# Optimization experiments

Hardware: AMD Instinct MI355X
Metric: run time of the kernel (lower is better)

## Reference

```python
import jax, jax.numpy as jnp
import numpy as np

N = 100000   # total nodes (users + items)
D = 256      # in_channels == out_channels
E = 1000000  # directed edges
C = 64       # number of clusters


def setup_inputs() -> dict:
    key = jax.random.key(0)
    k1, k2, k3, k4, k5 = jax.random.split(key, 5)
    X = jax.random.normal(k1, (N, D), jnp.float32)
    weight = jax.random.normal(k2, (D, D), jnp.float32) / np.sqrt(D).astype(np.float32)
    bias = jax.random.normal(k3, (D,), jnp.float32) * 0.01
    cluster_assignment = jax.random.randint(k4, (N,), 0, C)
    edge_index = jax.random.randint(k5, (2, E), 0, N)
    return {"X": X, "weight": weight, "bias": bias,
            "cluster_assignment": cluster_assignment, "edge_index": edge_index}


def reference(X, weight, bias, cluster_assignment, edge_index):
    # Per-cluster GCNConv == whole-graph GCNConv restricted to intra-cluster
    # edges (edges crossing clusters are masked out), with self-loops added
    # per node. Clusters with zero intra-cluster edges are skipped and keep
    # the original X (the Python loop `continue`s).
    src, dst = edge_index[0], edge_index[1]
    intra = (cluster_assignment[src] == cluster_assignment[dst]).astype(X.dtype)

    # GCN symmetric normalization with self-loops: deg = A_intra deg + 1
    deg = jax.ops.segment_sum(intra, dst, num_segments=N) + 1.0
    dinv = jax.lax.rsqrt(deg)                      # deg >= 1 always
    norm = dinv[src] * dinv[dst] * intra           # zero on cross-cluster edges

    Xl = X @ weight                                # [N, D] linear transform
    agg = jax.ops.segment_sum(norm[:, None] * Xl[src], dst, num_segments=N)
    agg = agg + (dinv * dinv)[:, None] * Xl        # self-loop contribution
    out = agg + bias

    # Clusters with no internal edges are left untouched by the torch loop.
    edges_per_cluster = jax.ops.segment_sum(intra, cluster_assignment[dst], num_segments=C)
    active = edges_per_cluster[cluster_assignment] > 0  # [N] bool
    return jnp.where(active[:, None], out, X)
```

## Files before the change

### kernel.cpp

```cpp
#include <hip/hip_runtime.h>

#define D 256

typedef float f32x4 __attribute__((ext_vector_type(4)));
typedef _Float16 f16x8 __attribute__((ext_vector_type(8)));

__global__ void k_prepw(const float* __restrict__ W, _Float16* __restrict__ Wp,
                        float* __restrict__ degx, int* __restrict__ activeC,
                        int* __restrict__ bcnt, int N) {
    int idx = blockIdx.x * blockDim.x + threadIdx.x;
    if (idx < N) degx[idx] = 0.0f;
    if (idx < 64) activeC[idx] = 0;
    if (idx < 256 * 32) bcnt[idx] = 0;
    if (idx >= D * D) return;
    int k = idx >> 8, n = idx & 255;
    int ks = k >> 5, kk = k & 31;
    int h = kk >> 3, i = kk & 7;
    int ct = n >> 4, cn = n & 15;
    int lane = h * 16 + cn;
    Wp[(((ks * 16 + ct) * 64 + lane) << 3) + i] = (_Float16)W[idx];
}

__global__ void k_edges(const int* __restrict__ ei, const int* __restrict__ cl,
                        float* __restrict__ degx, int2* __restrict__ elist,
                        int* __restrict__ bcnt, int E) {
    int e = blockIdx.x * blockDim.x + threadIdx.x;
    if (e >= E) return;
    int s = ei[e];
    int d = ei[E + e];
    if (cl[s] == cl[d]) {
        unsafeAtomicAdd(&degx[d], 1.0f);
        int b = blockIdx.x & 255;
        int pos = atomicAdd(&bcnt[b << 5], 1);
        if (pos < 256) elist[(b << 8) + pos] = make_int2(s, d);
    }
}

__global__ void k_init(const float* __restrict__ X, const float* __restrict__ degx,
                       const int* __restrict__ cl, int* __restrict__ activeC,
                       float* __restrict__ out, int N) {
    int i = blockIdx.x * blockDim.x + threadIdx.x;
    int lane = threadIdx.x & 63;
    float dx = 0.0f;
    bool hit = false;
    if (i < N) {
        dx = degx[i];
        hit = dx > 0.0f;
        if (hit) activeC[cl[i]] = 1;
    }
    unsigned long long m = __ballot(hit);
    int base = i - lane;
    while (m) {
        int b = __ffsll((long long)m) - 1;
        m &= m - 1;
        int r = base + b;
        float inv = 1.0f / (__shfl(dx, b) + 1.0f);
        float4 x = *(const float4*)(X + (size_t)r * D + lane * 4);
        x.x *= inv; x.y *= inv; x.z *= inv; x.w *= inv;
        *(float4*)(out + (size_t)r * D + lane * 4) = x;
    }
}

__global__ void k_scatter2(const int2* __restrict__ elist,
                           const int* __restrict__ bcnt,
                           const float* __restrict__ degx,
                           const float* __restrict__ X,
                           float* __restrict__ out) {
    int b = blockIdx.x >> 2;
    int w = ((blockIdx.x & 3) << 2) + (threadIdx.x >> 6);
    int lane = threadIdx.x & 63;
    int cnt = bcnt[b << 5];
    if (cnt > 256) cnt = 256;
    for (int i = w; i < cnt; i += 16) {
        int2 e = elist[(b << 8) + i];
        float norm = rsqrtf((degx[e.x] + 1.0f) * (degx[e.y] + 1.0f));
        float4 xv = *(const float4*)(X + (size_t)e.x * D + lane * 4);
        float* op = out + (size_t)e.y * D + lane * 4;
        unsafeAtomicAdd(op + 0, norm * xv.x);
        unsafeAtomicAdd(op + 1, norm * xv.y);
        unsafeAtomicAdd(op + 2, norm * xv.z);
        unsafeAtomicAdd(op + 3, norm * xv.w);
    }
}

__global__ __launch_bounds__(1024, 4) void k_gemm(
        const _Float16* __restrict__ Wp, const float* __restrict__ bias,
        const float* __restrict__ X, const float* __restrict__ degx,
        const int* __restrict__ cl, const int* __restrict__ activeC,
        float* __restrict__ out, int N) {
    extern __shared__ _Float16 Wl[];
    int tid  = threadIdx.x;
    int lane = tid & 63;
    int wid  = tid >> 6;
    int rA = lane & 15;
    int h  = lane >> 4;
    int cn = lane & 15;

    {
        const char* src = (const char*)Wp + tid * 16;
        #pragma unroll
        for (int it = 0; it < 8; ++it) {
            __builtin_amdgcn_global_load_lds(
                (const __attribute__((address_space(1))) void*)(src + it * 16384),
                (__attribute__((address_space(3))) void*)((char*)Wl + tid * 16 + it * 16384),
                16, 0, 0);
        }
    }
    float bv[16];
    #pragma unroll
    for (int ct = 0; ct < 16; ++ct) bv[ct] = bias[ct * 16 + cn];
    __syncthreads();

    int T = (N + 15) >> 4;
    for (int t = (int)blockIdx.x * 16 + wid; t < T; t += 4096) {
        long r = (long)t * 16 + rA;
        if (r > (long)N - 1) r = (long)N - 1;
        const float* arow = ((degx[r] > 0.0f) ? out : X) + r * D;

        f32x4 acc[16];
        #pragma unroll
        for (int ct = 0; ct < 16; ++ct) acc[ct] = (f32x4){0.f, 0.f, 0.f, 0.f};

        float4 Pa = *(const float4*)(arow + h * 8);
        float4 Pb = *(const float4*)(arow + h * 8 + 4);
        #pragma unroll
        for (int ks = 0; ks < 8; ++ks) {
            float4 a0 = Pa, a1 = Pb;
            if (ks < 7) {
                Pa = *(const float4*)(arow + (ks + 1) * 32 + h * 8);
                Pb = *(const float4*)(arow + (ks + 1) * 32 + h * 8 + 4);
            }
            f16x8 af;
            af[0]=(_Float16)a0.x; af[1]=(_Float16)a0.y; af[2]=(_Float16)a0.z; af[3]=(_Float16)a0.w;
            af[4]=(_Float16)a1.x; af[5]=(_Float16)a1.y; af[6]=(_Float16)a1.z; af[7]=(_Float16)a1.w;
            #pragma unroll
            for (int ct = 0; ct < 16; ++ct) {
                f16x8 wf = *(const f16x8*)&Wl[(((ks * 16 + ct) * 64) + lane) << 3];
                acc[ct] = __builtin_amdgcn_mfma_f32_16x16x32_f16(af, wf, acc[ct], 0, 0, 0);
            }
        }

        #pragma unroll
        for (int j = 0; j < 4; ++j) {
            long rr = (long)t * 16 + h * 4 + j;
            bool ok = rr < (long)N;
            long rc = ok ? rr : (long)N - 1;
            bool act = activeC[cl[rc]] != 0;
            unsigned long long bad = __ballot(!act || !ok);
            float* orow = out + rc * D;
            if (bad == 0ULL) {
                #pragma unroll
                for (int ct = 0; ct < 16; ++ct)
                    orow[ct * 16 + cn] = acc[ct][j] + bv[ct];
            } else if (ok) {
                const float* xrow = X + rc * D;
                #pragma unroll
                for (int ct = 0; ct < 16; ++ct) {
                    float v = acc[ct][j] + bv[ct];
                    if (!act) v = xrow[ct * 16 + cn];
                    orow[ct * 16 + cn] = v;
                }
            }
        }
    }
}

extern "C" void kernel_launch(void* const* d_in, const int* in_sizes, int n_in,
                              void* d_out, int out_size, void* d_ws, size_t ws_size,
                              hipStream_t stream) {
    const float* X    = (const float*)d_in[0];
    const float* W    = (const float*)d_in[1];
    const float* bias = (const float*)d_in[2];
    const int*   cl   = (const int*)d_in[3];
    const int*   ei   = (const int*)d_in[4];
    int N = in_sizes[3];
    int E = in_sizes[4] / 2;
    float* out = (float*)d_out;

    char* ws = (char*)d_ws;
    float* degx = (float*)ws;
    size_t off = ((size_t)N * sizeof(float) + 255) & ~(size_t)255;
    int* activeC = (int*)(ws + off);
    int* bcnt    = (int*)(ws + off + 256);
    int2* elist  = (int2*)(ws + off + 256 + 256 * 32 * sizeof(int));
    size_t off2 = off + 256 + 256 * 32 * sizeof(int) + 256 * 256 * sizeof(int2);
    _Float16* Wp = (_Float16*)(ws + ((off2 + 255) & ~(size_t)255));

    hipFuncSetAttribute((const void*)k_gemm,
                        hipFuncAttributeMaxDynamicSharedMemorySize, 131072);

    int npz = (N > D * D) ? N : D * D;
    k_prepw<<<(npz + 255) / 256, 256, 0, stream>>>(W, Wp, degx, activeC, bcnt, N);
    k_edges<<<(E + 255) / 256, 256, 0, stream>>>(ei, cl, degx, elist, bcnt, E);
    k_init<<<(N + 255) / 256, 256, 0, stream>>>(X, degx, cl, activeC, out, N);
    k_scatter2<<<1024, 256, 0, stream>>>(elist, bcnt, degx, X, out);
    k_gemm<<<256, 1024, 131072, stream>>>(Wp, bias, X, degx, cl, activeC, out, N);
}
```

Measured before the change: 128.9 us.

## Fuse all five stages into one cooperative kernel with grid-wide syncs

Merges the weight prep, edge filtering, init, edge scatter and GEMM stages into a single cooperative kernel launched with 256×1024 threads, separating phases with grid.sync(). Edge processing becomes a grid-stride loop, with the block id serving directly as the elist bucket. This aims to remove the launch overhead and inter-kernel gaps of five separate launches. In exchange, the memory-bound phases run at the lower occupancy that the GEMM's launch bounds and 128KB of LDS allow, and each grid barrier adds synchronisation cost.

```diff
diff --git a/kernel.cpp b/kernel.cpp
--- a/kernel.cpp
+++ b/kernel.cpp
@@ -1,102 +1,97 @@
 #include <hip/hip_runtime.h>
+#include <hip/hip_cooperative_groups.h>
 
 #define D 256
+
+namespace cg = cooperative_groups;
 
 typedef float f32x4 __attribute__((ext_vector_type(4)));
 typedef _Float16 f16x8 __attribute__((ext_vector_type(8)));
 
-__global__ void k_prepw(const float* __restrict__ W, _Float16* __restrict__ Wp,
-                        float* __restrict__ degx, int* __restrict__ activeC,
-                        int* __restrict__ bcnt, int N) {
-    int idx = blockIdx.x * blockDim.x + threadIdx.x;
-    if (idx < N) degx[idx] = 0.0f;
-    if (idx < 64) activeC[idx] = 0;
-    if (idx < 256 * 32) bcnt[idx] = 0;
-    if (idx >= D * D) return;
-    int k = idx >> 8, n = idx & 255;
-    int ks = k >> 5, kk = k & 31;
-    int h = kk >> 3, i = kk & 7;
-    int ct = n >> 4, cn = n & 15;
-    int lane = h * 16 + cn;
-    Wp[(((ks * 16 + ct) * 64 + lane) << 3) + i] = (_Float16)W[idx];
-}
+__global__ __launch_bounds__(1024, 4) void k_fused(
+        const float* __restrict__ W, const float* __restrict__ bias,
+        const float* __restrict__ X, const int* __restrict__ cl,
+        const int* __restrict__ ei, _Float16* __restrict__ Wp,
+        float* __restrict__ degx, int* __restrict__ activeC,
+        int* __restrict__ bcnt, int2* __restrict__ elist,
+        float* __restrict__ out, int E, int N) {
+    extern __shared__ _Float16 Wl[];
+    cg::grid_group grid = cg::this_grid();
+    const int tid  = threadIdx.x;
+    const int bid  = blockIdx.x;
+    const int gtid = bid * 1024 + tid;
+    const int lane = tid & 63;
 
-__global__ void k_edges(const int* __restrict__ ei, const int* __restrict__ cl,
-                        float* __restrict__ degx, int2* __restrict__ elist,
-                        int* __restrict__ bcnt, int E) {
-    int e = blockIdx.x * blockDim.x + threadIdx.x;
-    if (e >= E) return;
-    int s = ei[e];
-    int d = ei[E + e];
-    if (cl[s] == cl[d]) {
-        unsafeAtomicAdd(&degx[d], 1.0f);
-        int b = blockIdx.x & 255;
-        int pos = atomicAdd(&bcnt[b << 5], 1);
-        if (pos < 256) elist[(b << 8) + pos] = make_int2(s, d);
+    if (gtid < N) degx[gtid] = 0.0f;
+    if (gtid < 64) activeC[gtid] = 0;
+    if (gtid < 256 * 32) bcnt[gtid] = 0;
+    if (gtid < D * D) {
+        int k = gtid >> 8, n = gtid & 255;
+        int ks = k >> 5, kk = k & 31;
+        int h = kk >> 3, i = kk & 7;
+        int ct = n >> 4, cn = n & 15;
+        int ln = h * 16 + cn;
+        Wp[(((ks * 16 + ct) * 64 + ln) << 3) + i] = (_Float16)W[gtid];
     }
-}
+    grid.sync();
 
-__global__ void k_init(const float* __restrict__ X, const float* __restrict__ degx,
-                       const int* __restrict__ cl, int* __restrict__ activeC,
-                       float* __restrict__ out, int N) {
-    int i = blockIdx.x * blockDim.x + threadIdx.x;
-    int lane = threadIdx.x & 63;
-    float dx = 0.0f;
-    bool hit = false;
-    if (i < N) {
-        dx = degx[i];
-        hit = dx > 0.0f;
-        if (hit) activeC[cl[i]] = 1;
+    for (int e = gtid; e < E; e += 262144) {
+        int s = ei[e];
+        int d = ei[E + e];
+        if (cl[s] == cl[d]) {
+            unsafeAtomicAdd(&degx[d], 1.0f);
+            int pos = atomicAdd(&bcnt[bid << 5], 1);
+            if (pos < 256) elist[(bid << 8) + pos] = make_int2(s, d);
+        }
     }
-    unsigned long long m = __ballot(hit);
-    int base = i - lane;
-    while (m) {
-        int b = __ffsll((long long)m) - 1;
-        m &= m - 1;
-        int r = base + b;
-        float inv = 1.0f / (__shfl(dx, b) + 1.0f);
-        float4 x = *(const float4*)(X + (size_t)r * D + lane * 4);
-        x.x *= inv; x.y *= inv; x.z *= inv; x.w *= inv;
-        *(float4*)(out + (size_t)r * D + lane * 4) = x;
-    }
-}
-
-__global__ void k_scatter2(const int2* __restrict__ elist,
-                           const int* __restrict__ bcnt,
-                           const float* __restrict__ degx,
-                           const float* __restrict__ X,
-                           float* __restrict__ out) {
-    int b = blockIdx.x >> 2;
-    int w = ((blockIdx.x & 3) << 2) + (threadIdx.x >> 6);
-    int lane = threadIdx.x & 63;
-    int cnt = bcnt[b << 5];
-    if (cnt > 256) cnt = 256;
-    for (int i = w; i < cnt; i += 16) {
-        int2 e = elist[(b << 8) + i];
-        float norm = rsqrtf((degx[e.x] + 1.0f) * (degx[e.y] + 1.0f));
-        float4 xv = *(const float4*)(X + (size_t)e.x * D + lane * 4);
-        float* op = out + (size_t)e.y * D + lane * 4;
-        unsafeAtomicAdd(op + 0, norm * xv.x);
-        unsafeAtomicAdd(op + 1, norm * xv.y);
-        unsafeAtomicAdd(op + 2, norm * xv.z);
-        unsafeAtomicAdd(op + 3, norm * xv.w);
-    }
-}
-
-__global__ __launch_bounds__(1024, 4) void k_gemm(
-        const _Float16* __restrict__ Wp, const float* __restrict__ bias,
-        const float* __restrict__ X, const float* __restrict__ degx,
-        const int* __restrict__ cl, const int* __restrict__ activeC,
-        float* __restrict__ out, int N) {
-    extern __shared__ _Float16 Wl[];
-    int tid  = threadIdx.x;
-    int lane = tid & 63;
-    int wid  = tid >> 6;
-    int rA = lane & 15;
-    int h  = lane >> 4;
-    int cn = lane & 15;
+    grid.sync();
 
     {
+        int i = gtid;
+        float dx = 0.0f;
+        bool hit = false;
+        if (i < N) {
+            dx = degx[i];
+            hit = dx > 0.0f;
+            if (hit) activeC[cl[i]] = 1;
+        }
+        unsigned long long m = __ballot(hit);
+        int base = i - lane;
+        while (m) {
+            int b = __ffsll((long long)m) - 1;
+            m &= m - 1;
+            int r = base + b;
+            float inv = 1.0f / (__shfl(dx, b) + 1.0f);
+            float4 x = *(const float4*)(X + (size_t)r * D + lane * 4);
+            x.x *= inv; x.y *= inv; x.z *= inv; x.w *= inv;
+            *(float4*)(out + (size_t)r * D + lane * 4) = x;
+        }
+    }
+    grid.sync();
+
+    {
+        int w = tid >> 6;
+        int cnt = bcnt[bid << 5];
+        if (cnt > 256) cnt = 256;
+        for (int i = w; i < cnt; i += 16) {
+            int2 e = elist[(bid << 8) + i];
+            float norm = rsqrtf((degx[e.x] + 1.0f) * (degx[e.y] + 1.0f));
+            float4 xv = *(const float4*)(X + (size_t)e.x * D + lane * 4);
+            float* op = out + (size_t)e.y * D + lane * 4;
+            unsafeAtomicAdd(op + 0, norm * xv.x);
+            unsafeAtomicAdd(op + 1, norm * xv.y);
+            unsafeAtomicAdd(op + 2, norm * xv.z);
+            unsafeAtomicAdd(op + 3, norm * xv.w);
+        }
+    }
+    grid.sync();
+
+    {
+        int wid = tid >> 6;
+        int rA = lane & 15;
+        int h  = lane >> 4;
+        int cn = lane & 15;
+
         const char* src = (const char*)Wp + tid * 16;
         #pragma unroll
         for (int it = 0; it < 8; ++it) {
@@ -105,60 +100,60 @@
                 (__attribute__((address_space(3))) void*)((char*)Wl + tid * 16 + it * 16384),
                 16, 0, 0);
         }
-    }
-    float bv[16];
-    #pragma unroll
-    for (int ct = 0; ct < 16; ++ct) bv[ct] = bias[ct * 16 + cn];
-    __syncthreads();
+        float bv[16];
+        #pragma unroll
+        for (int ct = 0; ct < 16; ++ct) bv[ct] = bias[ct * 16 + cn];
+        __syncthreads();
 
-    int T = (N + 15) >> 4;
-    for (int t = (int)blockIdx.x * 16 + wid; t < T; t += 4096) {
-        long r = (long)t * 16 + rA;
-        if (r > (long)N - 1) r = (long)N - 1;
-        const float* arow = ((degx[r] > 0.0f) ? out : X) + r * D;
+        int T = (N + 15) >> 4;
+        for (int t = bid * 16 + wid; t < T; t += 4096) {
+            long r = (long)t * 16 + rA;
+            if (r > (long)N - 1) r = (long)N - 1;
+            const float* arow = ((degx[r] > 0.0f) ? out : X) + r * D;
 
-        f32x4 acc[16];
-        #pragma unroll
-        for (int ct = 0; ct < 16; ++ct) acc[ct] = (f32x4){0.f, 0.f, 0.f, 0.f};
+            f32x4 acc[16];
+            #pragma unroll
+            for (int ct = 0; ct < 16; ++ct) acc[ct] = (f32x4){0.f, 0.f, 0.f, 0.f};
 
-        float4 Pa = *(const float4*)(arow + h * 8);
-        float4 Pb = *(const float4*)(arow + h * 8 + 4);
-        #pragma unroll
-        for (int ks = 0; ks < 8; ++ks) {
-            float4 a0 = Pa, a1 = Pb;
-            if (ks < 7) {
-                Pa = *(const float4*)(arow + (ks + 1) * 32 + h * 8);
-                Pb = *(const float4*)(arow + (ks + 1) * 32 + h * 8 + 4);
-            }
-            f16x8 af;
-            af[0]=(_Float16)a0.x; af[1]=(_Float16)a0.y; af[2]=(_Float16)a0.z; af[3]=(_Float16)a0.w;
-            af[4]=(_Float16)a1.x; af[5]=(_Float16)a1.y; af[6]=(_Float16)a1.z; af[7]=(_Float16)a1.w;
+            float4 Pa = *(const float4*)(arow + h * 8);
+            float4 Pb = *(const float4*)(arow + h * 8 + 4);
             #pragma unroll
-            for (int ct = 0; ct < 16; ++ct) {
-                f16x8 wf = *(const f16x8*)&Wl[(((ks * 16 + ct) * 64) + lane) << 3];
-                acc[ct] = __builtin_amdgcn_mfma_f32_16x16x32_f16(af, wf, acc[ct], 0, 0, 0);
-            }
-        }
-
-        #pragma unroll
-        for (int j = 0; j < 4; ++j) {
-            long rr = (long)t * 16 + h * 4 + j;
-            bool ok = rr < (long)N;
-            long rc = ok ? rr : (long)N - 1;
-            bool act = activeC[cl[rc]] != 0;
-            unsigned long long bad = __ballot(!act || !ok);
-            float* orow = out + rc * D;
-            if (bad == 0ULL) {
-                #pragma unroll
-                for (int ct = 0; ct < 16; ++ct)
-                    orow[ct * 16 + cn] = acc[ct][j] + bv[ct];
-            } else if (ok) {
-                const float* xrow = X + rc * D;
+            for (int ks = 0; ks < 8; ++ks) {
+                float4 a0 = Pa, a1 = Pb;
+                if (ks < 7) {
+                    Pa = *(const float4*)(arow + (ks + 1) * 32 + h * 8);
+                    Pb = *(const float4*)(arow + (ks + 1) * 32 + h * 8 + 4);
+                }
+                f16x8 af;
+                af[0]=(_Float16)a0.x; af[1]=(_Float16)a0.y; af[2]=(_Float16)a0.z; af[3]=(_Float16)a0.w;
+                af[4]=(_Float16)a1.x; af[5]=(_Float16)a1.y; af[6]=(_Float16)a1.z; af[7]=(_Float16)a1.w;
                 #pragma unroll
                 for (int ct = 0; ct < 16; ++ct) {
-                    float v = acc[ct][j] + bv[ct];
-                    if (!act) v = xrow[ct * 16 + cn];
-                    orow[ct * 16 + cn] = v;
+                    f16x8 wf = *(const f16x8*)&Wl[(((ks * 16 + ct) * 64) + lane) << 3];
+                    acc[ct] = __builtin_amdgcn_mfma_f32_16x16x32_f16(af, wf, acc[ct], 0, 0, 0);
+                }
+            }
+
+            #pragma unroll
+            for (int j = 0; j < 4; ++j) {
+                long rr = (long)t * 16 + h * 4 + j;
+                bool ok = rr < (long)N;
+                long rc = ok ? rr : (long)N - 1;
+                bool act = activeC[cl[rc]] != 0;
+                unsigned long long bad = __ballot(!act || !ok);
+                float* orow = out + rc * D;
+                if (bad == 0ULL) {
+                    #pragma unroll
+                    for (int ct = 0; ct < 16; ++ct)
+                        orow[ct * 16 + cn] = acc[ct][j] + bv[ct];
+                } else if (ok) {
+                    const float* xrow = X + rc * D;
+                    #pragma unroll
+                    for (int ct = 0; ct < 16; ++ct) {
+                        float v = acc[ct][j] + bv[ct];
+                        if (!act) v = xrow[ct * 16 + cn];
+                        orow[ct * 16 + cn] = v;
+                    }
                 }
             }
         }
@@ -186,13 +181,12 @@
     size_t off2 = off + 256 + 256 * 32 * sizeof(int) + 256 * 256 * sizeof(int2);
     _Float16* Wp = (_Float16*)(ws + ((off2 + 255) & ~(size_t)255));
 
-    hipFuncSetAttribute((const void*)k_gemm,
+    hipFuncSetAttribute((const void*)k_fused,
                         hipFuncAttributeMaxDynamicSharedMemorySize, 131072);
 
-    int npz = (N > D * D) ? N : D * D;
-    k_prepw<<<(npz + 255) / 256, 256, 0, stream>>>(W, Wp, degx, activeC, bcnt, N);
-    k_edges<<<(E + 255) / 256, 256, 0, stream>>>(ei, cl, degx, elist, bcnt, E);
-    k_init<<<(N + 255) / 256, 256, 0, stream>>>(X, degx, cl, activeC, out, N);
-    k_scatter2<<<1024, 256, 0, stream>>>(elist, bcnt, degx, X, out);
-    k_gemm<<<256, 1024, 131072, stream>>>(Wp, bias, X, degx, cl, activeC, out, N);
+    void* args[] = { (void*)&W, (void*)&bias, (void*)&X, (void*)&cl, (void*)&ei,
+                     (void*)&Wp, (void*)&degx, (void*)&activeC, (void*)&bcnt,
+                     (void*)&elist, (void*)&out, (void*)&E, (void*)&N };
+    hipLaunchCooperativeKernel((const void*)k_fused, dim3(256), dim3(1024),
+                               args, 131072, stream);
 }
```

New measurement: 244.6 us. 1.9x slower.
